# Performance work log

Measured on AMD Instinct MI355X. Metric: run time of the kernel, lower is better.

## Reference

```python
import jax, jax.numpy as jnp
import numpy as np

B, D = 65536, 512
E_SPEC, E_SH = 2, 2
H1, H2, EO, TH = 64, 32, 32, 64
T1_DIM, T2_DIM = 3, 2


def _lin(key, shape, fan_in):
    bound = 1.0 / np.sqrt(fan_in)
    return jax.random.uniform(key, shape, jnp.float32, -bound, bound)


def _expert_params(key, n):
    ks = jax.random.split(key, 6)
    return (
        _lin(ks[0], (n, D, H1), D), _lin(ks[1], (n, H1), D),
        _lin(ks[2], (n, H1, H2), H1), _lin(ks[3], (n, H2), H1),
        _lin(ks[4], (n, H2, EO), H2), _lin(ks[5], (n, EO), H2),
    )


def setup_inputs() -> dict:
    key = jax.random.key(0)
    ks = jax.random.split(key, 8)
    x = jax.random.normal(ks[0], (B, D), jnp.float32)
    sh = _expert_params(ks[1], E_SH)
    t1 = _expert_params(ks[2], E_SPEC)
    t2 = _expert_params(ks[3], E_SPEC)
    EG = E_SPEC + E_SH
    g1_W, g1_b = _lin(jax.random.fold_in(ks[4], 0), (D, EG), D), _lin(jax.random.fold_in(ks[4], 1), (EG,), D)
    g2_W, g2_b = _lin(jax.random.fold_in(ks[5], 0), (D, EG), D), _lin(jax.random.fold_in(ks[5], 1), (EG,), D)
    kt = jax.random.split(ks[6], 4)
    tw1_W1, tw1_b1 = _lin(kt[0], (EO, TH), EO), _lin(kt[1], (TH,), EO)
    tw1_W2, tw1_b2 = _lin(kt[2], (TH, T1_DIM), TH), _lin(kt[3], (T1_DIM,), TH)
    kt2 = jax.random.split(ks[7], 4)
    tw2_W1, tw2_b1 = _lin(kt2[0], (EO, TH), EO), _lin(kt2[1], (TH,), EO)
    tw2_W2, tw2_b2 = _lin(kt2[2], (TH, T2_DIM), TH), _lin(kt2[3], (T2_DIM,), TH)
    return {
        "x": x,
        "sh_W1": sh[0], "sh_b1": sh[1], "sh_W2": sh[2], "sh_b2": sh[3], "sh_W3": sh[4], "sh_b3": sh[5],
        "t1_W1": t1[0], "t1_b1": t1[1], "t1_W2": t1[2], "t1_b2": t1[3], "t1_W3": t1[4], "t1_b3": t1[5],
        "t2_W1": t2[0], "t2_b1": t2[1], "t2_W2": t2[2], "t2_b2": t2[3], "t2_W3": t2[4], "t2_b3": t2[5],
        "g1_W": g1_W, "g1_b": g1_b, "g2_W": g2_W, "g2_b": g2_b,
        "tw1_W1": tw1_W1, "tw1_b1": tw1_b1, "tw1_W2": tw1_W2, "tw1_b2": tw1_b2,
        "tw2_W1": tw2_W1, "tw2_b1": tw2_b1, "tw2_W2": tw2_W2, "tw2_b2": tw2_b2,
    }


def _experts(x, W1, b1, W2, b2, W3, b3):
    # batched over expert dim e: [e, B, h] (dropout is identity in eval)
    h = jax.nn.relu(jnp.einsum('bi,eih->ebh', x, W1) + b1[:, None, :])
    h = jax.nn.relu(jnp.einsum('ebh,ehk->ebk', h, W2) + b2[:, None, :])
    return jnp.einsum('ebk,eko->ebo', h, W3) + b3[:, None, :]


def _tower(g, W1, b1, W2, b2):
    return jax.nn.relu(g @ W1 + b1) @ W2 + b2


def reference(x, sh_W1, sh_b1, sh_W2, sh_b2, sh_W3, sh_b3,
              t1_W1, t1_b1, t1_W2, t1_b2, t1_W3, t1_b3,
              t2_W1, t2_b1, t2_W2, t2_b2, t2_W3, t2_b3,
              g1_W, g1_b, g2_W, g2_b,
              tw1_W1, tw1_b1, tw1_W2, tw1_b2,
              tw2_W1, tw2_b1, tw2_W2, tw2_b2):
    shared = _experts(x, sh_W1, sh_b1, sh_W2, sh_b2, sh_W3, sh_b3)   # [E_SH, B, EO]
    task1 = _experts(x, t1_W1, t1_b1, t1_W2, t1_b2, t1_W3, t1_b3)    # [E_SPEC, B, EO]
    task2 = _experts(x, t2_W1, t2_b1, t2_W2, t2_b2, t2_W3, t2_b3)

    sel1 = jax.nn.softmax(x @ g1_W + g1_b, axis=1)                    # [B, E_SPEC+E_SH]
    g1 = jnp.einsum('ebc,be->bc', jnp.concatenate([task1, shared], 0), sel1)
    o1 = _tower(g1, tw1_W1, tw1_b1, tw1_W2, tw1_b2)
    o1 = o1.at[:, 0].set(jax.nn.sigmoid(o1[:, 0]))
    o1 = o1.at[:, 2].set(jax.nn.sigmoid(o1[:, 2]))

    sel2 = jax.nn.softmax(x @ g2_W + g2_b, axis=1)
    g2 = jnp.einsum('ebc,be->bc', jnp.concatenate([task2, shared], 0), sel2)
    o2 = _tower(g2, tw2_W1, tw2_b1, tw2_W2, tw2_b2)
    o2 = o2.at[:, 1].set(jax.nn.sigmoid(o2[:, 1]))
    return (o1, o2)
```

## Files before the change

kernel.cpp:

```cpp
#include <hip/hip_runtime.h>
#include <hip/hip_bf16.h>


#define MT 32
#define NT1 25

typedef __bf16 bf16x8 __attribute__((ext_vector_type(8)));
typedef float f32x4 __attribute__((ext_vector_type(4)));

__device__ __forceinline__ unsigned short f2bf(float f) {
    unsigned u = __builtin_bit_cast(unsigned, f);
    return (unsigned short)((u + 0x7FFFu + ((u >> 16) & 1u)) >> 16);
}
__device__ __forceinline__ unsigned pk(float a, float b) {
    return (unsigned)f2bf(a) | ((unsigned)f2bf(b) << 16);
}

__global__ void pack_all(const float* __restrict__ sh_W1, const float* __restrict__ t1_W1,
                         const float* __restrict__ t2_W1, const float* __restrict__ g1_W,
                         const float* __restrict__ g2_W,
                         const float* __restrict__ sh_W2, const float* __restrict__ t1_W2,
                         const float* __restrict__ t2_W2,
                         const float* __restrict__ sh_W3, const float* __restrict__ t1_W3,
                         const float* __restrict__ t2_W3,
                         const float* __restrict__ sh_b1, const float* __restrict__ t1_b1,
                         const float* __restrict__ t2_b1,
                         const float* __restrict__ sh_b2, const float* __restrict__ t1_b2,
                         const float* __restrict__ t2_b2,
                         const float* __restrict__ sh_b3, const float* __restrict__ t1_b3,
                         const float* __restrict__ t2_b3,
                         const float* __restrict__ g1_b, const float* __restrict__ g2_b,
                         unsigned short* __restrict__ wf1, unsigned short* __restrict__ wf2,
                         unsigned short* __restrict__ wf3,
                         float* __restrict__ b1c, float* __restrict__ b2c, float* __restrict__ b3c) {
    int p0 = blockIdx.x * blockDim.x + threadIdx.x;
    if (p0 < 204800) {
        int p = p0;
        int j = p & 7, lane = (p >> 3) & 63, ks = (p >> 9) & 15, nt = p >> 13;
        int col = nt * 16 + (lane & 15);
        int k = ks * 32 + (lane >> 4) * 8 + j;
        float v = 0.f;
        if (col < 384) {
            int e = col >> 6, ci = col & 63;
            const float* W = (e < 2) ? t1_W1 : (e < 4) ? t2_W1 : sh_W1;
            v = W[((size_t)(e & 1) * 512 + k) * 64 + ci];
        } else if (col < 388) {
            v = g1_W[k * 4 + (col - 384)];
        } else if (col < 392) {
            v = g2_W[k * 4 + (col - 388)];
        }
        wf1[p] = f2bf(v);
        return;
    }
    int p = p0 - 204800;
    if (p < 12288) {
        int j = p & 7, lane = (p >> 3) & 63, ks = (p >> 9) & 1, nt = (p >> 10) & 1, e = p >> 11;
        int col = nt * 16 + (lane & 15);
        int k = ks * 32 + (lane >> 4) * 8 + j;
        const float* W = (e < 2) ? t1_W2 : (e < 4) ? t2_W2 : sh_W2;
        wf2[p] = f2bf(W[((size_t)(e & 1) * 64 + k) * 32 + col]);
    } else if (p < 18432) {
        int q = p - 12288;
        int j = q & 7, lane = (q >> 3) & 63, nt = (q >> 9) & 1, e = q >> 10;
        int col = nt * 16 + (lane & 15);
        int k = (lane >> 4) * 8 + j;
        const float* W = (e < 2) ? t1_W3 : (e < 4) ? t2_W3 : sh_W3;
        wf3[q] = f2bf(W[((size_t)(e & 1) * 32 + k) * 32 + col]);
    } else if (p < 18432 + 392) {
        int t = p - 18432;
        float v;
        if (t < 384) {
            int e = t >> 6, ci = t & 63;
            const float* bb = (e < 2) ? t1_b1 : (e < 4) ? t2_b1 : sh_b1;
            v = bb[(e & 1) * 64 + ci];
        } else if (t < 388) v = g1_b[t - 384];
        else v = g2_b[t - 388];
        b1c[t] = v;
    } else if (p < 18824 + 192) {
        int t = p - 18824;
        int e = t >> 5, ci = t & 31;
        const float* bb = (e < 2) ? t1_b2 : (e < 4) ? t2_b2 : sh_b2;
        b2c[t] = bb[(e & 1) * 32 + ci];
    } else if (p < 19016 + 192) {
        int t = p - 19016;
        int e = t >> 5, ci = t & 31;
        const float* bb = (e < 2) ? t1_b3 : (e < 4) ? t2_b3 : sh_b3;
        b3c[t] = bb[(e & 1) * 32 + ci];
    }
}

#define LDS_BYTES 74240

__global__ __launch_bounds__(512, 4) void ple_fused(
    const float* __restrict__ x,
    const unsigned short* __restrict__ wf1, const unsigned short* __restrict__ wf2,
    const unsigned short* __restrict__ wf3,
    const float* __restrict__ b1c, const float* __restrict__ b2c, const float* __restrict__ b3c,
    const float* __restrict__ tw1_W1, const float* __restrict__ tw1_b1,
    const float* __restrict__ tw1_W2, const float* __restrict__ tw1_b2,
    const float* __restrict__ tw2_W1, const float* __restrict__ tw2_b1,
    const float* __restrict__ tw2_W2, const float* __restrict__ tw2_b2,
    float* __restrict__ out, int ntok) {
    extern __shared__ char smem[];
    unsigned short* xlds = (unsigned short*)smem;
    float* g1l = (float*)(smem + 0);
    float* g2l = (float*)(smem + 4224);
    float* th1 = (float*)(smem + 8448);
    float* th2 = (float*)(smem + 16896);
    unsigned short* h1 = (unsigned short*)(smem + 33280);
    float* eo = (float*)(smem + 33280);
    unsigned short* h2 = (unsigned short*)(smem + 59392);
    float* gate = (float*)(smem + 72192);
    float* sel = (float*)(smem + 73216);

    const int tid = threadIdx.x;
    const int w = tid >> 6, l = tid & 63, r = l & 15, g = l >> 4;
    const int tok0 = blockIdx.x * MT;

    const float* xb = x + (size_t)tok0 * 512;
#pragma unroll
    for (int i = 0; i < 4; ++i) {
        int f = i * 4096 + tid * 8;
        const float4 a = *(const float4*)(xb + f);
        const float4 b = *(const float4*)(xb + f + 4);
        int tok = f >> 9, k = f & 511;
        uint4 u = make_uint4(pk(a.x, a.y), pk(a.z, a.w), pk(b.x, b.y), pk(b.z, b.w));
        *(uint4*)(&xlds[tok * 520 + k]) = u;
    }
    __syncthreads();

    int ntl[4] = {w, w + 8, w + 16, 24};
    const int ntn = (w == 7) ? 4 : 3;

    f32x4 acc[4][2];
#pragma unroll
    for (int i = 0; i < 4; ++i)
#pragma unroll
        for (int m = 0; m < 2; ++m) acc[i][m] = (f32x4){0.f, 0.f, 0.f, 0.f};

    const bf16x8* wf1v = (const bf16x8*)wf1;
#pragma unroll 4
    for (int ks = 0; ks < 16; ++ks) {
        bf16x8 bfr[4];
#pragma unroll
        for (int i = 0; i < 4; ++i)
            if (i < ntn) bfr[i] = wf1v[((ntl[i] * 16 + ks) << 6) + l];
        bf16x8 afr[2];
#pragma unroll
        for (int m = 0; m < 2; ++m)
            afr[m] = *(const bf16x8*)&xlds[(m * 16 + r) * 520 + ks * 32 + g * 8];
#pragma unroll
        for (int i = 0; i < 4; ++i)
            if (i < ntn)
#pragma unroll
                for (int m = 0; m < 2; ++m)
                    acc[i][m] = __builtin_amdgcn_mfma_f32_16x16x32_bf16(afr[m], bfr[i], acc[i][m], 0, 0, 0);
    }

#pragma unroll
    for (int i = 0; i < 4; ++i)
        if (i < ntn) {
            int nt = ntl[i];
            if (nt < 24) {
#pragma unroll
                for (int m = 0; m < 2; ++m)
#pragma unroll
                    for (int q = 0; q < 4; ++q) {
                        int tokr = m * 16 + g * 4 + q;
                        int col = nt * 16 + r;
                        float v = acc[i][m][q] + b1c[col];
                        h1[tokr * 408 + col] = f2bf(fmaxf(v, 0.f));
                    }
            } else if (r < 8) {
#pragma unroll
                for (int m = 0; m < 2; ++m)
#pragma unroll
                    for (int q = 0; q < 4; ++q) {
                        int tokr = m * 16 + g * 4 + q;
                        gate[tokr * 8 + r] = acc[i][m][q] + b1c[384 + r];
                    }
            }
        }
    __syncthreads();

    if (tid < 32) {
#pragma unroll
        for (int gi = 0; gi < 2; ++gi) {
            float l0 = gate[tid * 8 + gi * 4 + 0];
            float l1 = gate[tid * 8 + gi * 4 + 1];
            float l2 = gate[tid * 8 + gi * 4 + 2];
            float l3 = gate[tid * 8 + gi * 4 + 3];
            float mx = fmaxf(fmaxf(l0, l1), fmaxf(l2, l3));
            float e0 = __expf(l0 - mx), e1 = __expf(l1 - mx);
            float e2 = __expf(l2 - mx), e3 = __expf(l3 - mx);
            float inv = 1.f / (e0 + e1 + e2 + e3);
            sel[tid * 8 + gi * 4 + 0] = e0 * inv;
            sel[tid * 8 + gi * 4 + 1] = e1 * inv;
            sel[tid * 8 + gi * 4 + 2] = e2 * inv;
            sel[tid * 8 + gi * 4 + 3] = e3 * inv;
        }
    }

    const int nj = (w < 4) ? 2 : 1;
    const int je[2] = {w >> 1, (w + 8) >> 1};
    const int jn[2] = {w & 1, w & 1};

    f32x4 acc2[2][2];
#pragma unroll
    for (int jj = 0; jj < 2; ++jj)
#pragma unroll
        for (int m = 0; m < 2; ++m) acc2[jj][m] = (f32x4){0.f, 0.f, 0.f, 0.f};

    const bf16x8* wf2v = (const bf16x8*)wf2;
#pragma unroll
    for (int jj = 0; jj < 2; ++jj)
        if (jj < nj) {
            int e = je[jj], nt2 = jn[jj];
#pragma unroll
            for (int ks = 0; ks < 2; ++ks) {
                bf16x8 bb = wf2v[(((e * 2 + nt2) * 2 + ks) << 6) + l];
#pragma unroll
                for (int m = 0; m < 2; ++m) {
                    bf16x8 aa = *(const bf16x8*)&h1[(m * 16 + r) * 408 + e * 64 + ks * 32 + g * 8];
                    acc2[jj][m] = __builtin_amdgcn_mfma_f32_16x16x32_bf16(aa, bb, acc2[jj][m], 0, 0, 0);
                }
            }
        }
#pragma unroll
    for (int jj = 0; jj < 2; ++jj)
        if (jj < nj) {
            int e = je[jj], nt2 = jn[jj];
#pragma unroll
            for (int m = 0; m < 2; ++m)
#pragma unroll
                for (int q = 0; q < 4; ++q) {
                    int tokr = m * 16 + g * 4 + q;
                    int col = nt2 * 16 + r;
                    float v = acc2[jj][m][q] + b2c[e * 32 + col];
                    h2[tokr * 200 + e * 32 + col] = f2bf(fmaxf(v, 0.f));
                }
        }
    __syncthreads();

    f32x4 acc3[2][2];
#pragma unroll
    for (int jj = 0; jj < 2; ++jj)
#pragma unroll
        for (int m = 0; m < 2; ++m) acc3[jj][m] = (f32x4){0.f, 0.f, 0.f, 0.f};

    const bf16x8* wf3v = (const bf16x8*)wf3;
#pragma unroll
    for (int jj = 0; jj < 2; ++jj)
        if (jj < nj) {
            int e = je[jj], nt2 = jn[jj];
            bf16x8 bb = wf3v[((e * 2 + nt2) << 6) + l];
#pragma unroll
            for (int m = 0; m < 2; ++m) {
                bf16x8 aa = *(const bf16x8*)&h2[(m * 16 + r) * 200 + e * 32 + g * 8];
                acc3[jj][m] = __builtin_amdgcn_mfma_f32_16x16x32_bf16(aa, bb, acc3[jj][m], 0, 0, 0);
            }
        }
#pragma unroll
    for (int jj = 0; jj < 2; ++jj)
        if (jj < nj) {
            int e = je[jj], nt2 = jn[jj];
#pragma unroll
            for (int m = 0; m < 2; ++m)
#pragma unroll
                for (int q = 0; q < 4; ++q) {
                    int tokr = m * 16 + g * 4 + q;
                    eo[(e * 32 + tokr) * 33 + nt2 * 16 + r] =
                        acc3[jj][m][q] + b3c[e * 32 + nt2 * 16 + r];
                }
        }
    __syncthreads();

    {
        int tok = tid >> 4, c0 = (tid & 15) * 2;
        float s[8];
#pragma unroll
        for (int i = 0; i < 8; ++i) s[i] = sel[tok * 8 + i];
#pragma unroll
        for (int c = 0; c < 2; ++c) {
            int cc = c0 + c;
            float e0 = eo[(0 * 32 + tok) * 33 + cc];
            float e1 = eo[(1 * 32 + tok) * 33 + cc];
            float e2 = eo[(2 * 32 + tok) * 33 + cc];
            float e3 = eo[(3 * 32 + tok) * 33 + cc];
            float e4 = eo[(4 * 32 + tok) * 33 + cc];
            float e5 = eo[(5 * 32 + tok) * 33 + cc];
            g1l[tok * 33 + cc] = s[0] * e0 + s[1] * e1 + s[2] * e4 + s[3] * e5;
            g2l[tok * 33 + cc] = s[4] * e2 + s[5] * e3 + s[6] * e4 + s[7] * e5;
        }
    }
    __syncthreads();

    {
        int t = tid & 255, tower = tid >> 8;
        int tok = t >> 3, h0 = (t & 7) * 8;
        const float* W1 = tower ? tw2_W1 : tw1_W1;
        const float* B1 = tower ? tw2_b1 : tw1_b1;
        const float* gl = tower ? g2l : g1l;
        float* th = tower ? th2 : th1;
        float a[8];
#pragma unroll
        for (int hh = 0; hh < 8; ++hh) a[hh] = B1[h0 + hh];
        for (int c = 0; c < 32; ++c) {
            float gv = gl[tok * 33 + c];
#pragma unroll
            for (int hh = 0; hh < 8; ++hh)
                a[hh] += gv * W1[c * 64 + h0 + hh];
        }
#pragma unroll
        for (int hh = 0; hh < 8; ++hh)
            th[tok * 66 + h0 + hh] = fmaxf(a[hh], 0.f);
    }
    __syncthreads();

    if (tid < 128) {
        int tok = tid >> 2, jx = tid & 3;
        if (jx < 3) {
            float s = tw1_b2[jx];
            for (int hh = 0; hh < 64; ++hh) s += th1[tok * 66 + hh] * tw1_W2[hh * 3 + jx];
            if (jx != 1) s = 1.f / (1.f + __expf(-s));
            out[(size_t)(tok0 + tok) * 3 + jx] = s;
        }
    } else if (tid >= 256 && tid < 384) {
        int t = tid - 256, tok = t >> 2, jx = t & 3;
        if (jx < 2) {
            float s = tw2_b2[jx];
            for (int hh = 0; hh < 64; ++hh) s += th2[tok * 66 + hh] * tw2_W2[hh * 2 + jx];
            if (jx == 1) s = 1.f / (1.f + __expf(-s));
            out[(size_t)ntok * 3 + (size_t)(tok0 + tok) * 2 + jx] = s;
        }
    }
}

extern "C" void kernel_launch(void* const* d_in, const int* in_sizes, int n_in,
                              void* d_out, int out_size, void* d_ws, size_t ws_size,
                              hipStream_t stream) {
    const float* x = (const float*)d_in[0];
    const float* sh_W1 = (const float*)d_in[1];
    const float* sh_b1 = (const float*)d_in[2];
    const float* sh_W2 = (const float*)d_in[3];
    const float* sh_b2 = (const float*)d_in[4];
    const float* sh_W3 = (const float*)d_in[5];
    const float* sh_b3 = (const float*)d_in[6];
    const float* t1_W1 = (const float*)d_in[7];
    const float* t1_b1 = (const float*)d_in[8];
    const float* t1_W2 = (const float*)d_in[9];
    const float* t1_b2 = (const float*)d_in[10];
    const float* t1_W3 = (const float*)d_in[11];
    const float* t1_b3 = (const float*)d_in[12];
    const float* t2_W1 = (const float*)d_in[13];
    const float* t2_b1 = (const float*)d_in[14];
    const float* t2_W2 = (const float*)d_in[15];
    const float* t2_b2 = (const float*)d_in[16];
    const float* t2_W3 = (const float*)d_in[17];
    const float* t2_b3 = (const float*)d_in[18];
    const float* g1_W = (const float*)d_in[19];
    const float* g1_b = (const float*)d_in[20];
    const float* g2_W = (const float*)d_in[21];
    const float* g2_b = (const float*)d_in[22];
    const float* tw1_W1 = (const float*)d_in[23];
    const float* tw1_b1 = (const float*)d_in[24];
    const float* tw1_W2 = (const float*)d_in[25];
    const float* tw1_b2 = (const float*)d_in[26];
    const float* tw2_W1 = (const float*)d_in[27];
    const float* tw2_b1 = (const float*)d_in[28];
    const float* tw2_W2 = (const float*)d_in[29];
    const float* tw2_b2 = (const float*)d_in[30];

    unsigned short* wf1 = (unsigned short*)d_ws;
    unsigned short* wf2 = (unsigned short*)((char*)d_ws + 409600);
    unsigned short* wf3 = (unsigned short*)((char*)d_ws + 434176);
    float* b1c = (float*)((char*)d_ws + 446464);
    float* b2c = (float*)((char*)d_ws + 448032);
    float* b3c = (float*)((char*)d_ws + 448800);

    pack_all<<<438, 512, 0, stream>>>(sh_W1, t1_W1, t2_W1, g1_W, g2_W,
                                      sh_W2, t1_W2, t2_W2, sh_W3, t1_W3, t2_W3,
                                      sh_b1, t1_b1, t2_b1, sh_b2, t1_b2, t2_b2,
                                      sh_b3, t1_b3, t2_b3, g1_b, g2_b,
                                      wf1, wf2, wf3, b1c, b2c, b3c);

    (void)hipFuncSetAttribute((const void*)ple_fused,
                              hipFuncAttributeMaxDynamicSharedMemorySize, LDS_BYTES);

    int ntok = in_sizes[0] / 512;
    int nblk = ntok / MT;
    ple_fused<<<nblk, 512, LDS_BYTES, stream>>>(
        x, wf1, wf2, wf3, b1c, b2c, b3c,
        tw1_W1, tw1_b1, tw1_W2, tw1_b2, tw2_W1, tw2_b1, tw2_W2, tw2_b2,
        (float*)d_out, ntok);
}
```

Before: 306.9 us.

## Make fused PLE kernel persistent with register prefetch of next x tile

The kernel now launches a fixed grid of 512 blocks. Each block loops over several 32-token tiles instead of handling a single tile per block. While the current tile computes, the next tile's x rows are loaded into registers, hiding global memory latency behind MFMA work. The tower and gate buffers were moved in LDS so they no longer overlap the x staging area, which the next iteration overwrites. This adds 32 live float registers under tight launch bounds, which risks spills. The loop also assumes the token count divides evenly by 32*512.

```diff
diff --git a/kernel.cpp b/kernel.cpp
--- a/kernel.cpp
+++ b/kernel.cpp
@@ -4,6 +4,7 @@
 
 #define MT 32
 #define NT1 25
+#define NBLK 512
 
 typedef __bf16 bf16x8 __attribute__((ext_vector_type(8)));
 typedef float f32x4 __attribute__((ext_vector_type(4)));
@@ -103,235 +104,257 @@
     float* __restrict__ out, int ntok) {
     extern __shared__ char smem[];
     unsigned short* xlds = (unsigned short*)smem;
-    float* g1l = (float*)(smem + 0);
-    float* g2l = (float*)(smem + 4224);
-    float* th1 = (float*)(smem + 8448);
-    float* th2 = (float*)(smem + 16896);
     unsigned short* h1 = (unsigned short*)(smem + 33280);
     float* eo = (float*)(smem + 33280);
+    float* th1 = (float*)(smem + 33280);
+    float* th2 = (float*)(smem + 41728);
     unsigned short* h2 = (unsigned short*)(smem + 59392);
+    float* g1l = (float*)(smem + 59392);
+    float* g2l = (float*)(smem + 63616);
     float* gate = (float*)(smem + 72192);
     float* sel = (float*)(smem + 73216);
 
     const int tid = threadIdx.x;
     const int w = tid >> 6, l = tid & 63, r = l & 15, g = l >> 4;
-    const int tok0 = blockIdx.x * MT;
-
-    const float* xb = x + (size_t)tok0 * 512;
+
+    const int ntiles = ntok / (MT * NBLK);
+
+    float4 pre[8];
 #pragma unroll
     for (int i = 0; i < 4; ++i) {
-        int f = i * 4096 + tid * 8;
-        const float4 a = *(const float4*)(xb + f);
-        const float4 b = *(const float4*)(xb + f + 4);
-        int tok = f >> 9, k = f & 511;
-        uint4 u = make_uint4(pk(a.x, a.y), pk(a.z, a.w), pk(b.x, b.y), pk(b.z, b.w));
-        *(uint4*)(&xlds[tok * 520 + k]) = u;
+        const float* xb = x + ((size_t)blockIdx.x * MT) * 512 + i * 4096 + tid * 8;
+        pre[2 * i] = *(const float4*)xb;
+        pre[2 * i + 1] = *(const float4*)(xb + 4);
     }
-    __syncthreads();
-
-    int ntl[4] = {w, w + 8, w + 16, 24};
-    const int ntn = (w == 7) ? 4 : 3;
-
-    f32x4 acc[4][2];
-#pragma unroll
-    for (int i = 0; i < 4; ++i)
-#pragma unroll
-        for (int m = 0; m < 2; ++m) acc[i][m] = (f32x4){0.f, 0.f, 0.f, 0.f};
-
-    const bf16x8* wf1v = (const bf16x8*)wf1;
+
+#pragma unroll 1
+    for (int t = 0; t < ntiles; ++t) {
+        const int tok0 = (blockIdx.x + t * NBLK) * MT;
+
+#pragma unroll
+        for (int i = 0; i < 4; ++i) {
+            int f = i * 4096 + tid * 8;
+            int tok = f >> 9, k = f & 511;
+            float4 a = pre[2 * i], b = pre[2 * i + 1];
+            *(uint4*)(&xlds[tok * 520 + k]) =
+                make_uint4(pk(a.x, a.y), pk(a.z, a.w), pk(b.x, b.y), pk(b.z, b.w));
+        }
+        __syncthreads();
+
+        if (t + 1 < ntiles) {
+#pragma unroll
+            for (int i = 0; i < 4; ++i) {
+                const float* xb = x + ((size_t)(blockIdx.x + (t + 1) * NBLK) * MT) * 512
+                                  + i * 4096 + tid * 8;
+                pre[2 * i] = *(const float4*)xb;
+                pre[2 * i + 1] = *(const float4*)(xb + 4);
+            }
+        }
+
+        int ntl[4] = {w, w + 8, w + 16, 24};
+        const int ntn = (w == 7) ? 4 : 3;
+
+        f32x4 acc[4][2];
+#pragma unroll
+        for (int i = 0; i < 4; ++i)
+#pragma unroll
+            for (int m = 0; m < 2; ++m) acc[i][m] = (f32x4){0.f, 0.f, 0.f, 0.f};
+
+        const bf16x8* wf1v = (const bf16x8*)wf1;
 #pragma unroll 4
-    for (int ks = 0; ks < 16; ++ks) {
-        bf16x8 bfr[4];
+        for (int ks = 0; ks < 16; ++ks) {
+            bf16x8 bfr[4];
+#pragma unroll
+            for (int i = 0; i < 4; ++i)
+                if (i < ntn) bfr[i] = wf1v[((ntl[i] * 16 + ks) << 6) + l];
+            bf16x8 afr[2];
+#pragma unroll
+            for (int m = 0; m < 2; ++m)
+                afr[m] = *(const bf16x8*)&xlds[(m * 16 + r) * 520 + ks * 32 + g * 8];
+#pragma unroll
+            for (int i = 0; i < 4; ++i)
+                if (i < ntn)
+#pragma unroll
+                    for (int m = 0; m < 2; ++m)
+                        acc[i][m] = __builtin_amdgcn_mfma_f32_16x16x32_bf16(afr[m], bfr[i], acc[i][m], 0, 0, 0);
+        }
+
 #pragma unroll
         for (int i = 0; i < 4; ++i)
-            if (i < ntn) bfr[i] = wf1v[((ntl[i] * 16 + ks) << 6) + l];
-        bf16x8 afr[2];
-#pragma unroll
-        for (int m = 0; m < 2; ++m)
-            afr[m] = *(const bf16x8*)&xlds[(m * 16 + r) * 520 + ks * 32 + g * 8];
-#pragma unroll
-        for (int i = 0; i < 4; ++i)
-            if (i < ntn)
-#pragma unroll
-                for (int m = 0; m < 2; ++m)
-                    acc[i][m] = __builtin_amdgcn_mfma_f32_16x16x32_bf16(afr[m], bfr[i], acc[i][m], 0, 0, 0);
-    }
-
-#pragma unroll
-    for (int i = 0; i < 4; ++i)
-        if (i < ntn) {
-            int nt = ntl[i];
-            if (nt < 24) {
+            if (i < ntn) {
+                int nt = ntl[i];
+                if (nt < 24) {
+#pragma unroll
+                    for (int m = 0; m < 2; ++m)
+#pragma unroll
+                        for (int q = 0; q < 4; ++q) {
+                            int tokr = m * 16 + g * 4 + q;
+                            int col = nt * 16 + r;
+                            float v = acc[i][m][q] + b1c[col];
+                            h1[tokr * 408 + col] = f2bf(fmaxf(v, 0.f));
+                        }
+                } else if (r < 8) {
+#pragma unroll
+                    for (int m = 0; m < 2; ++m)
+#pragma unroll
+                        for (int q = 0; q < 4; ++q) {
+                            int tokr = m * 16 + g * 4 + q;
+                            gate[tokr * 8 + r] = acc[i][m][q] + b1c[384 + r];
+                        }
+                }
+            }
+        __syncthreads();
+
+        if (tid < 32) {
+#pragma unroll
+            for (int gi = 0; gi < 2; ++gi) {
+                float l0 = gate[tid * 8 + gi * 4 + 0];
+                float l1 = gate[tid * 8 + gi * 4 + 1];
+                float l2 = gate[tid * 8 + gi * 4 + 2];
+                float l3 = gate[tid * 8 + gi * 4 + 3];
+                float mx = fmaxf(fmaxf(l0, l1), fmaxf(l2, l3));
+                float e0 = __expf(l0 - mx), e1 = __expf(l1 - mx);
+                float e2 = __expf(l2 - mx), e3 = __expf(l3 - mx);
+                float inv = 1.f / (e0 + e1 + e2 + e3);
+                sel[tid * 8 + gi * 4 + 0] = e0 * inv;
+                sel[tid * 8 + gi * 4 + 1] = e1 * inv;
+                sel[tid * 8 + gi * 4 + 2] = e2 * inv;
+                sel[tid * 8 + gi * 4 + 3] = e3 * inv;
+            }
+        }
+
+        const int nj = (w < 4) ? 2 : 1;
+        const int je[2] = {w >> 1, (w + 8) >> 1};
+        const int jn[2] = {w & 1, w & 1};
+
+        f32x4 acc2[2][2];
+#pragma unroll
+        for (int jj = 0; jj < 2; ++jj)
+#pragma unroll
+            for (int m = 0; m < 2; ++m) acc2[jj][m] = (f32x4){0.f, 0.f, 0.f, 0.f};
+
+        const bf16x8* wf2v = (const bf16x8*)wf2;
+#pragma unroll
+        for (int jj = 0; jj < 2; ++jj)
+            if (jj < nj) {
+                int e = je[jj], nt2 = jn[jj];
+#pragma unroll
+                for (int ks = 0; ks < 2; ++ks) {
+                    bf16x8 bb = wf2v[(((e * 2 + nt2) * 2 + ks) << 6) + l];
+#pragma unroll
+                    for (int m = 0; m < 2; ++m) {
+                        bf16x8 aa = *(const bf16x8*)&h1[(m * 16 + r) * 408 + e * 64 + ks * 32 + g * 8];
+                        acc2[jj][m] = __builtin_amdgcn_mfma_f32_16x16x32_bf16(aa, bb, acc2[jj][m], 0, 0, 0);
+                    }
+                }
+            }
+#pragma unroll
+        for (int jj = 0; jj < 2; ++jj)
+            if (jj < nj) {
+                int e = je[jj], nt2 = jn[jj];
 #pragma unroll
                 for (int m = 0; m < 2; ++m)
 #pragma unroll
                     for (int q = 0; q < 4; ++q) {
                         int tokr = m * 16 + g * 4 + q;
-                        int col = nt * 16 + r;
-                        float v = acc[i][m][q] + b1c[col];
-                        h1[tokr * 408 + col] = f2bf(fmaxf(v, 0.f));
+                        int col = nt2 * 16 + r;
+                        float v = acc2[jj][m][q] + b2c[e * 32 + col];
+                        h2[tokr * 200 + e * 32 + col] = f2bf(fmaxf(v, 0.f));
                     }
-            } else if (r < 8) {
+            }
+        __syncthreads();
+
+        f32x4 acc3[2][2];
+#pragma unroll
+        for (int jj = 0; jj < 2; ++jj)
+#pragma unroll
+            for (int m = 0; m < 2; ++m) acc3[jj][m] = (f32x4){0.f, 0.f, 0.f, 0.f};
+
+        const bf16x8* wf3v = (const bf16x8*)wf3;
+#pragma unroll
+        for (int jj = 0; jj < 2; ++jj)
+            if (jj < nj) {
+                int e = je[jj], nt2 = jn[jj];
+                bf16x8 bb = wf3v[((e * 2 + nt2) << 6) + l];
+#pragma unroll
+                for (int m = 0; m < 2; ++m) {
+                    bf16x8 aa = *(const bf16x8*)&h2[(m * 16 + r) * 200 + e * 32 + g * 8];
+                    acc3[jj][m] = __builtin_amdgcn_mfma_f32_16x16x32_bf16(aa, bb, acc3[jj][m], 0, 0, 0);
+                }
+            }
+#pragma unroll
+        for (int jj = 0; jj < 2; ++jj)
+            if (jj < nj) {
+                int e = je[jj], nt2 = jn[jj];
 #pragma unroll
                 for (int m = 0; m < 2; ++m)
 #pragma unroll
                     for (int q = 0; q < 4; ++q) {
                         int tokr = m * 16 + g * 4 + q;
-                        gate[tokr * 8 + r] = acc[i][m][q] + b1c[384 + r];
+                        eo[(e * 32 + tokr) * 33 + nt2 * 16 + r] =
+                            acc3[jj][m][q] + b3c[e * 32 + nt2 * 16 + r];
                     }
             }
-        }
-    __syncthreads();
-
-    if (tid < 32) {
-#pragma unroll
-        for (int gi = 0; gi < 2; ++gi) {
-            float l0 = gate[tid * 8 + gi * 4 + 0];
-            float l1 = gate[tid * 8 + gi * 4 + 1];
-            float l2 = gate[tid * 8 + gi * 4 + 2];
-            float l3 = gate[tid * 8 + gi * 4 + 3];
-            float mx = fmaxf(fmaxf(l0, l1), fmaxf(l2, l3));
-            float e0 = __expf(l0 - mx), e1 = __expf(l1 - mx);
-            float e2 = __expf(l2 - mx), e3 = __expf(l3 - mx);
-            float inv = 1.f / (e0 + e1 + e2 + e3);
-            sel[tid * 8 + gi * 4 + 0] = e0 * inv;
-            sel[tid * 8 + gi * 4 + 1] = e1 * inv;
-            sel[tid * 8 + gi * 4 + 2] = e2 * inv;
-            sel[tid * 8 + gi * 4 + 3] = e3 * inv;
-        }
-    }
-
-    const int nj = (w < 4) ? 2 : 1;
-    const int je[2] = {w >> 1, (w + 8) >> 1};
-    const int jn[2] = {w & 1, w & 1};
-
-    f32x4 acc2[2][2];
-#pragma unroll
-    for (int jj = 0; jj < 2; ++jj)
-#pragma unroll
-        for (int m = 0; m < 2; ++m) acc2[jj][m] = (f32x4){0.f, 0.f, 0.f, 0.f};
-
-    const bf16x8* wf2v = (const bf16x8*)wf2;
-#pragma unroll
-    for (int jj = 0; jj < 2; ++jj)
-        if (jj < nj) {
-            int e = je[jj], nt2 = jn[jj];
-#pragma unroll
-            for (int ks = 0; ks < 2; ++ks) {
-                bf16x8 bb = wf2v[(((e * 2 + nt2) * 2 + ks) << 6) + l];
-#pragma unroll
-                for (int m = 0; m < 2; ++m) {
-                    bf16x8 aa = *(const bf16x8*)&h1[(m * 16 + r) * 408 + e * 64 + ks * 32 + g * 8];
-                    acc2[jj][m] = __builtin_amdgcn_mfma_f32_16x16x32_bf16(aa, bb, acc2[jj][m], 0, 0, 0);
-                }
-            }
-        }
-#pragma unroll
-    for (int jj = 0; jj < 2; ++jj)
-        if (jj < nj) {
-            int e = je[jj], nt2 = jn[jj];
-#pragma unroll
-            for (int m = 0; m < 2; ++m)
-#pragma unroll
-                for (int q = 0; q < 4; ++q) {
-                    int tokr = m * 16 + g * 4 + q;
-                    int col = nt2 * 16 + r;
-                    float v = acc2[jj][m][q] + b2c[e * 32 + col];
-                    h2[tokr * 200 + e * 32 + col] = f2bf(fmaxf(v, 0.f));
-                }
-        }
-    __syncthreads();
-
-    f32x4 acc3[2][2];
-#pragma unroll
-    for (int jj = 0; jj < 2; ++jj)
-#pragma unroll
-        for (int m = 0; m < 2; ++m) acc3[jj][m] = (f32x4){0.f, 0.f, 0.f, 0.f};
-
-    const bf16x8* wf3v = (const bf16x8*)wf3;
-#pragma unroll
-    for (int jj = 0; jj < 2; ++jj)
-        if (jj < nj) {
-            int e = je[jj], nt2 = jn[jj];
-            bf16x8 bb = wf3v[((e * 2 + nt2) << 6) + l];
-#pragma unroll
-            for (int m = 0; m < 2; ++m) {
-                bf16x8 aa = *(const bf16x8*)&h2[(m * 16 + r) * 200 + e * 32 + g * 8];
-                acc3[jj][m] = __builtin_amdgcn_mfma_f32_16x16x32_bf16(aa, bb, acc3[jj][m], 0, 0, 0);
-            }
-        }
-#pragma unroll
-    for (int jj = 0; jj < 2; ++jj)
-        if (jj < nj) {
-            int e = je[jj], nt2 = jn[jj];
-#pragma unroll
-            for (int m = 0; m < 2; ++m)
-#pragma unroll
-                for (int q = 0; q < 4; ++q) {
-                    int tokr = m * 16 + g * 4 + q;
-                    eo[(e * 32 + tokr) * 33 + nt2 * 16 + r] =
-                        acc3[jj][m][q] + b3c[e * 32 + nt2 * 16 + r];
-                }
-        }
-    __syncthreads();
-
-    {
-        int tok = tid >> 4, c0 = (tid & 15) * 2;
-        float s[8];
-#pragma unroll
-        for (int i = 0; i < 8; ++i) s[i] = sel[tok * 8 + i];
-#pragma unroll
-        for (int c = 0; c < 2; ++c) {
-            int cc = c0 + c;
-            float e0 = eo[(0 * 32 + tok) * 33 + cc];
-            float e1 = eo[(1 * 32 + tok) * 33 + cc];
-            float e2 = eo[(2 * 32 + tok) * 33 + cc];
-            float e3 = eo[(3 * 32 + tok) * 33 + cc];
-            float e4 = eo[(4 * 32 + tok) * 33 + cc];
-            float e5 = eo[(5 * 32 + tok) * 33 + cc];
-            g1l[tok * 33 + cc] = s[0] * e0 + s[1] * e1 + s[2] * e4 + s[3] * e5;
-            g2l[tok * 33 + cc] = s[4] * e2 + s[5] * e3 + s[6] * e4 + s[7] * e5;
-        }
-    }
-    __syncthreads();
-
-    {
-        int t = tid & 255, tower = tid >> 8;
-        int tok = t >> 3, h0 = (t & 7) * 8;
-        const float* W1 = tower ? tw2_W1 : tw1_W1;
-        const float* B1 = tower ? tw2_b1 : tw1_b1;
-        const float* gl = tower ? g2l : g1l;
-        float* th = tower ? th2 : th1;
-        float a[8];
-#pragma unroll
-        for (int hh = 0; hh < 8; ++hh) a[hh] = B1[h0 + hh];
-        for (int c = 0; c < 32; ++c) {
-            float gv = gl[tok * 33 + c];
+        __syncthreads();
+
+        {
+            int tok = tid >> 4, c0 = (tid & 15) * 2;
+            float s[8];
+#pragma unroll
+            for (int i = 0; i < 8; ++i) s[i] = sel[tok * 8 + i];
+#pragma unroll
+            for (int c = 0; c < 2; ++c) {
+                int cc = c0 + c;
+                float e0 = eo[(0 * 32 + tok) * 33 + cc];
+                float e1 = eo[(1 * 32 + tok) * 33 + cc];
+                float e2 = eo[(2 * 32 + tok) * 33 + cc];
+                float e3 = eo[(3 * 32 + tok) * 33 + cc];
+                float e4 = eo[(4 * 32 + tok) * 33 + cc];
+                float e5 = eo[(5 * 32 + tok) * 33 + cc];
+                g1l[tok * 33 + cc] = s[0] * e0 + s[1] * e1 + s[2] * e4 + s[3] * e5;
+                g2l[tok * 33 + cc] = s[4] * e2 + s[5] * e3 + s[6] * e4 + s[7] * e5;
+            }
+        }
+        __syncthreads();
+
+        {
+            int tt = tid & 255, tower = tid >> 8;
+            int tok = tt >> 3, h0 = (tt & 7) * 8;
+            const float* W1 = tower ? tw2_W1 : tw1_W1;
+            const float* B1 = tower ? tw2_b1 : tw1_b1;
+            const float* gl = tower ? g2l : g1l;
+            float* th = tower ? th2 : th1;
+            float a[8];
+#pragma unroll
+            for (int hh = 0; hh < 8; ++hh) a[hh] = B1[h0 + hh];
+            for (int c = 0; c < 32; ++c) {
+                float gv = gl[tok * 33 + c];
+#pragma unroll
+                for (int hh = 0; hh < 8; ++hh)
+                    a[hh] += gv * W1[c * 64 + h0 + hh];
+            }
 #pragma unroll
             for (int hh = 0; hh < 8; ++hh)
-                a[hh] += gv * W1[c * 64 + h0 + hh];
-        }
-#pragma unroll
-        for (int hh = 0; hh < 8; ++hh)
-            th[tok * 66 + h0 + hh] = fmaxf(a[hh], 0.f);
-    }
-    __syncthreads();
-
-    if (tid < 128) {
-        int tok = tid >> 2, jx = tid & 3;
-        if (jx < 3) {
-            float s = tw1_b2[jx];
-            for (int hh = 0; hh < 64; ++hh) s += th1[tok * 66 + hh] * tw1_W2[hh * 3 + jx];
-            if (jx != 1) s = 1.f / (1.f + __expf(-s));
-            out[(size_t)(tok0 + tok) * 3 + jx] = s;
-        }
-    } else if (tid >= 256 && tid < 384) {
-        int t = tid - 256, tok = t >> 2, jx = t & 3;
-        if (jx < 2) {
-            float s = tw2_b2[jx];
-            for (int hh = 0; hh < 64; ++hh) s += th2[tok * 66 + hh] * tw2_W2[hh * 2 + jx];
-            if (jx == 1) s = 1.f / (1.f + __expf(-s));
-            out[(size_t)ntok * 3 + (size_t)(tok0 + tok) * 2 + jx] = s;
+                th[tok * 66 + h0 + hh] = fmaxf(a[hh], 0.f);
+        }
+        __syncthreads();
+
+        if (tid < 128) {
+            int tok = tid >> 2, jx = tid & 3;
+            if (jx < 3) {
+                float s = tw1_b2[jx];
+                for (int hh = 0; hh < 64; ++hh) s += th1[tok * 66 + hh] * tw1_W2[hh * 3 + jx];
+                if (jx != 1) s = 1.f / (1.f + __expf(-s));
+                out[(size_t)(tok0 + tok) * 3 + jx] = s;
+            }
+        } else if (tid >= 256 && tid < 384) {
+            int t2 = tid - 256, tok = t2 >> 2, jx = t2 & 3;
+            if (jx < 2) {
+                float s = tw2_b2[jx];
+                for (int hh = 0; hh < 64; ++hh) s += th2[tok * 66 + hh] * tw2_W2[hh * 2 + jx];
+                if (jx == 1) s = 1.f / (1.f + __expf(-s));
+                out[(size_t)ntok * 3 + (size_t)(tok0 + tok) * 2 + jx] = s;
+            }
         }
     }
 }
@@ -388,8 +411,7 @@
                               hipFuncAttributeMaxDynamicSharedMemorySize, LDS_BYTES);
 
     int ntok = in_sizes[0] / 512;
-    int nblk = ntok / MT;
-    ple_fused<<<nblk, 512, LDS_BYTES, stream>>>(
+    ple_fused<<<NBLK, 512, LDS_BYTES, stream>>>(
         x, wf1, wf2, wf3, b1c, b2c, b3c,
         tw1_W1, tw1_b1, tw1_W2, tw1_b2, tw2_W1, tw2_b1, tw2_W2, tw2_b2,
         (float*)d_out, ntok);
```

Result: slower. 378.0 us (+23.2%).
